# Kernel optimization log

Hardware: AMD Instinct MI355X
Metric: run time of the kernel (lower is better)

The kernel has to match this reference:

```python
import jax, jax.numpy as jnp
import numpy as np

N, IN_F, OUT_F, G = 8192, 1024, 1024, 5


def setup_inputs() -> dict:
    key = jax.random.key(0)
    k1, k2 = jax.random.split(key)
    x = jax.random.normal(k1, (N, IN_F), dtype=jnp.float32)
    spline_weights = jax.random.normal(k2, (OUT_F, IN_F, G), dtype=jnp.float32) * 0.1
    return {"x": x, "spline_weights": spline_weights}


def reference(x, spline_weights):
    out_f, in_f, g = spline_weights.shape
    grid = jnp.linspace(-1.0, 1.0, g).astype(x.dtype)
    leading = x.shape[:-1]
    xf = x.reshape(-1, in_f)                       # [N, in]
    x_c = jnp.clip(jnp.tanh(xf), grid[0], grid[-1])
    # bucket index: number of grid points <= x_c, minus 1, clamped to [0, g-2]
    idx = jnp.sum(x_c[..., None] >= grid, axis=-1) - 1
    idx = jnp.clip(idx, 0, g - 2)                  # [N, in] int
    idx_r = jnp.minimum(idx + 1, g - 1)
    g_left = grid[idx]
    g_right = grid[idx_r]
    t = (x_c - g_left) / (g_right - g_left + 1e-8)  # [N, in]
    # sparse interpolation coefficients over the grid axis: two nonzeros per (n,i)
    oh_l = jax.nn.one_hot(idx, g, dtype=xf.dtype)   # [N, in, G]
    oh_r = jax.nn.one_hot(idx_r, g, dtype=xf.dtype)
    coeff = (1.0 - t)[..., None] * oh_l + t[..., None] * oh_r  # [N, in, G]
    # y[n,o] = sum_i (1-t) * W[o,i,idx] + t * W[o,i,idx+1]
    out = jnp.einsum('nig,oig->no', coeff, spline_weights)
    return out.reshape(*leading, out_f)
```

## Files before the change

kernel.cpp:

```cpp
#include <hip/hip_runtime.h>
#include <stdint.h>

#define N_ROWS 8192
#define IN_F   1024
#define OUT_F  1024
#define NG     5
#define KTOT   (IN_F * NG)

typedef float          f32x4 __attribute__((ext_vector_type(4)));
typedef short          s16x8 __attribute__((ext_vector_type(8)));
typedef unsigned short u16x8 __attribute__((ext_vector_type(8)));

__device__ __forceinline__ unsigned short f2bf_rne(float f) {
    unsigned u = __float_as_uint(f);
    u = (u + 0x7fffu + ((u >> 16) & 1u)) >> 16;
    return (unsigned short)u;
}
__device__ __forceinline__ float bf2f(unsigned short h) {
    return __uint_as_float(((unsigned)h) << 16);
}
__device__ __forceinline__ void gload_lds16(const void* g, void* l) {
    __builtin_amdgcn_global_load_lds(
        (const __attribute__((address_space(1))) unsigned int*)g,
        (__attribute__((address_space(3))) unsigned int*)l, 16, 0, 0);
}

__global__ __launch_bounds__(256) void prep_a(const float* __restrict__ x,
                                              unsigned short* __restrict__ Ahp,
                                              unsigned short* __restrict__ Alp) {
    int t = blockIdx.x * 256 + threadIdx.x;
    int n = t >> 7, i8 = t & 127;
    const float4* xp = reinterpret_cast<const float4*>(x + (size_t)n * IN_F + i8 * 8);
    float4 a = xp[0], b = xp[1];
    float r[8] = {a.x, a.y, a.z, a.w, b.x, b.y, b.z, b.w};
    float xc[8];
#pragma unroll
    for (int j = 0; j < 8; ++j) {
        float v = fminf(fmaxf(r[j], -9.0f), 9.0f);
        float e = __expf(2.0f * v);
        xc[j] = (e - 1.0f) / (e + 1.0f);
    }
    size_t base = (size_t)n * KTOT + i8 * 8;
#pragma unroll
    for (int g = 0; g < NG; ++g) {
        float gv = -1.0f + 0.5f * (float)g;
        u16x8 hv, lv;
#pragma unroll
        for (int j = 0; j < 8; ++j) {
            float c  = fmaxf(0.0f, fmaf(-2.0f, fabsf(xc[j] - gv), 1.0f));
            unsigned hb = __float_as_uint(c) >> 16;
            hv[j] = (unsigned short)hb;
            lv[j] = (unsigned short)(__float_as_uint(c - __uint_as_float(hb << 16)) >> 16);
        }
        *reinterpret_cast<u16x8*>(&Ahp[base + g * 1024]) = hv;
        *reinterpret_cast<u16x8*>(&Alp[base + g * 1024]) = lv;
    }
}

__global__ __launch_bounds__(256) void prep_w(const float* __restrict__ W,
                                              unsigned short* __restrict__ Wh,
                                              unsigned short* __restrict__ Wl) {
    int t  = blockIdx.x * 256 + threadIdx.x;
    int o  = t >> 8, i4 = (t & 255) * 4;
    const float4* wp = reinterpret_cast<const float4*>(W + (size_t)o * KTOT + i4 * NG);
    float f[20];
#pragma unroll
    for (int q = 0; q < 5; ++q) {
        float4 v = wp[q];
        f[q*4+0] = v.x; f[q*4+1] = v.y; f[q*4+2] = v.z; f[q*4+3] = v.w;
    }
#pragma unroll
    for (int g = 0; g < NG; ++g) {
        ushort4 hq, lq;
        unsigned short* hp = (unsigned short*)&hq;
        unsigned short* lp = (unsigned short*)&lq;
#pragma unroll
        for (int di = 0; di < 4; ++di) {
            float w = f[di * NG + g];
            unsigned short h = f2bf_rne(w);
            hp[di] = h;
            lp[di] = f2bf_rne(w - bf2f(h));
        }
        int dst = o * KTOT + g * 1024 + i4;
        *reinterpret_cast<ushort4*>(&Wh[dst]) = hq;
        *reinterpret_cast<ushort4*>(&Wl[dst]) = lq;
    }
}

#define BM 128
#define BN 128
#define PBK 32
#define PNKT (KTOT / PBK)

struct SLdsDB { unsigned short d[2][4][BM * PBK]; };

__global__ __launch_bounds__(256, 2) void kan_gemm_pure(
        const unsigned short* __restrict__ Ahp,
        const unsigned short* __restrict__ Alp,
        const unsigned short* __restrict__ Wh,
        const unsigned short* __restrict__ Wl,
        float* __restrict__ out) {
    __shared__ SLdsDB s;

    int bid = blockIdx.x;
    int wg  = (bid & 7) * 64 + (bid >> 3);
    int nb  = wg >> 6;
    int mb  = wg & 63;
    int n0 = mb * BM, o0 = nb * BN;

    int tid  = threadIdx.x;
    int lane = tid & 63, wid = tid >> 6;
    int wm = wid >> 1, wn = wid & 1;

    int ks = (lane & 3) ^ ((lane >> 3) & 3);
    int gA[2], gB[2], ldsb[2];
#pragma unroll
    for (int q = 0; q < 2; ++q) {
        int r = wid * 32 + q * 16 + (lane >> 2);
        gA[q] = (n0 + r) * KTOT + ks * 8;
        gB[q] = (o0 + r) * KTOT + ks * 8;
        ldsb[q] = (wid * 32 + q * 16) * PBK;
    }
    int sl0  = lane >> 4;
    int arow = wm * 64 + (lane & 15);
    int brow = wn * 64 + (lane & 15);
    int aaddr = arow * PBK + ((sl0 ^ ((arow >> 1) & 3)) << 3);
    int baddr = brow * PBK + ((sl0 ^ ((brow >> 1) & 3)) << 3);

    f32x4 acc[4][4] = {};

    auto STAGE = [&](int buf, int k0) {
#pragma unroll
        for (int q = 0; q < 2; ++q) {
            gload_lds16(Ahp + gA[q] + k0, &s.d[buf][0][ldsb[q]]);
            gload_lds16(Alp + gA[q] + k0, &s.d[buf][1][ldsb[q]]);
            gload_lds16(Wh  + gB[q] + k0, &s.d[buf][2][ldsb[q]]);
            gload_lds16(Wl  + gB[q] + k0, &s.d[buf][3][ldsb[q]]);
        }
    };
    auto COMPUTE = [&](int buf) {
        s16x8 ah[4], al[4], bh[4], bl[4];
#pragma unroll
        for (int m = 0; m < 4; ++m) {
            ah[m] = *reinterpret_cast<const s16x8*>(&s.d[buf][0][aaddr + m * 512]);
            al[m] = *reinterpret_cast<const s16x8*>(&s.d[buf][1][aaddr + m * 512]);
        }
#pragma unroll
        for (int nf = 0; nf < 4; ++nf) {
            bh[nf] = *reinterpret_cast<const s16x8*>(&s.d[buf][2][baddr + nf * 512]);
            bl[nf] = *reinterpret_cast<const s16x8*>(&s.d[buf][3][baddr + nf * 512]);
        }
#pragma unroll
        for (int m = 0; m < 4; ++m)
#pragma unroll
            for (int nf = 0; nf < 4; ++nf) {
                acc[m][nf] = __builtin_amdgcn_mfma_f32_16x16x32_bf16(
                                 ah[m], bh[nf], acc[m][nf], 0, 0, 0);
                acc[m][nf] = __builtin_amdgcn_mfma_f32_16x16x32_bf16(
                                 ah[m], bl[nf], acc[m][nf], 0, 0, 0);
                acc[m][nf] = __builtin_amdgcn_mfma_f32_16x16x32_bf16(
                                 al[m], bh[nf], acc[m][nf], 0, 0, 0);
            }
    };

    STAGE(0, 0);
    __syncthreads();
    int cur = 0;
    for (int kt = 0; kt < PNKT - 1; ++kt) {
        STAGE(cur ^ 1, (kt + 1) * PBK);
        COMPUTE(cur);
        __syncthreads();
        cur ^= 1;
    }
    COMPUTE(cur);

    int rb = n0 + wm * 64 + (lane >> 4) * 4;
    int cb = o0 + wn * 64 + (lane & 15);
#pragma unroll
    for (int m = 0; m < 4; ++m)
#pragma unroll
        for (int nf = 0; nf < 4; ++nf)
#pragma unroll
            for (int jj = 0; jj < 4; ++jj)
                out[(size_t)(rb + m * 16 + jj) * OUT_F + cb + nf * 16] =
                    acc[m][nf][jj];
}

__global__ __launch_bounds__(256) void prep_p(const float* __restrict__ x,
                                              unsigned short* __restrict__ P) {
    int t = blockIdx.x * 256 + threadIdx.x;
    float4 a = reinterpret_cast<const float4*>(x)[t * 2];
    float4 b = reinterpret_cast<const float4*>(x)[t * 2 + 1];
    float r[8] = {a.x, a.y, a.z, a.w, b.x, b.y, b.z, b.w};
    u16x8 o;
#pragma unroll
    for (int j = 0; j < 8; ++j) {
        float xc = fminf(fmaxf(r[j], -9.0f), 9.0f);
        float e  = __expf(2.0f * xc);
        float th = (e - 1.0f) / (e + 1.0f);
        o[j] = (unsigned short)__float2uint_rn((th + 1.0f) * 32767.0f);
    }
    *reinterpret_cast<u16x8*>(&P[(size_t)t * 8]) = o;
}

#define MBM 64
#define MBN 256
#define MBK 32
struct SLdsM {
    unsigned short Ah[4 * MBM * 8];
    unsigned short Al[4 * MBM * 8];
    unsigned short Bh[4 * MBN * 8];
    unsigned short Bl[4 * MBN * 8];
};

__global__ __launch_bounds__(256, 3) void kan_gemm_mid(
        const unsigned short* __restrict__ P,
        const unsigned short* __restrict__ Wh,
        const unsigned short* __restrict__ Wl,
        float* __restrict__ out) {
    __shared__ SLdsM s;
    int bid = blockIdx.x;
    int wg  = (bid & 7) * 64 + (bid >> 3);
    int nb  = wg >> 7, mb = wg & 127;
    int n0 = mb * MBM, o0 = nb * MBN;
    int tid  = threadIdx.x;
    int lane = tid & 63, w = tid >> 6;

    int arow = tid >> 2, aks = tid & 3;
    int agoff = (n0 + arow) * IN_F + aks * 8;
    int aldst = aks * (MBM * 8) + arow * 8;
    int brow4 = tid >> 2, bchunk = tid & 3;
    int bldst = bchunk * (MBN * 8) + brow4 * 8;
    int bgq[4];
#pragma unroll
    for (int q = 0; q < 4; ++q)
        bgq[q] = (o0 + q * 64 + brow4) * KTOT + bchunk * 8;
    int fchunk = lane >> 4, fr = lane & 15;

    f32x4 acc[4][4] = {};
    for (int kt = 0; kt < KTOT / MBK; ++kt) {
        int k0 = kt * MBK;
        float gv = -1.0f + 0.5f * (float)(kt >> 5);
        int i0 = (kt & 31) * MBK;
        __syncthreads();
        u16x8 bregh[4], bregl[4];
#pragma unroll
        for (int q = 0; q < 4; ++q)
            bregh[q] = *reinterpret_cast<const u16x8*>(&Wh[bgq[q] + k0]);
#pragma unroll
        for (int q = 0; q < 4; ++q)
            bregl[q] = *reinterpret_cast<const u16x8*>(&Wl[bgq[q] + k0]);
        {
            u16x8 u = *reinterpret_cast<const u16x8*>(&P[agoff + i0]);
            u16x8 hv, lv;
#pragma unroll
            for (int j = 0; j < 8; ++j) {
                float xc = fmaf((float)u[j], (1.0f / 32767.0f), -1.0f);
                float c  = fmaxf(0.0f, fmaf(-2.0f, fabsf(xc - gv), 1.0f));
                unsigned hb = __float_as_uint(c) >> 16;
                hv[j] = (unsigned short)hb;
                lv[j] = (unsigned short)(__float_as_uint(c - __uint_as_float(hb << 16)) >> 16);
            }
            *reinterpret_cast<u16x8*>(&s.Ah[aldst]) = hv;
            *reinterpret_cast<u16x8*>(&s.Al[aldst]) = lv;
        }
#pragma unroll
        for (int q = 0; q < 4; ++q) {
            *reinterpret_cast<u16x8*>(&s.Bh[bldst + q * 512]) = bregh[q];
            *reinterpret_cast<u16x8*>(&s.Bl[bldst + q * 512]) = bregl[q];
        }
        __syncthreads();

        s16x8 ah[4], al[4], bh[4], bl[4];
#pragma unroll
        for (int m = 0; m < 4; ++m) {
            int e = fchunk * (MBM * 8) + (m * 16 + fr) * 8;
            ah[m] = *reinterpret_cast<const s16x8*>(&s.Ah[e]);
            al[m] = *reinterpret_cast<const s16x8*>(&s.Al[e]);
        }
#pragma unroll
        for (int nf = 0; nf < 4; ++nf) {
            int e = fchunk * (MBN * 8) + (w * 64 + nf * 16 + fr) * 8;
            bh[nf] = *reinterpret_cast<const s16x8*>(&s.Bh[e]);
            bl[nf] = *reinterpret_cast<const s16x8*>(&s.Bl[e]);
        }
#pragma unroll
        for (int m = 0; m < 4; ++m)
#pragma unroll
            for (int nf = 0; nf < 4; ++nf) {
                acc[m][nf] = __builtin_amdgcn_mfma_f32_16x16x32_bf16(
                                 ah[m], bh[nf], acc[m][nf], 0, 0, 0);
                acc[m][nf] = __builtin_amdgcn_mfma_f32_16x16x32_bf16(
                                 ah[m], bl[nf], acc[m][nf], 0, 0, 0);
                acc[m][nf] = __builtin_amdgcn_mfma_f32_16x16x32_bf16(
                                 al[m], bh[nf], acc[m][nf], 0, 0, 0);
            }
    }
    int rb = n0 + (lane >> 4) * 4;
    int cb = o0 + w * 64 + (lane & 15);
#pragma unroll
    for (int m = 0; m < 4; ++m)
#pragma unroll
        for (int nf = 0; nf < 4; ++nf)
#pragma unroll
            for (int jj = 0; jj < 4; ++jj)
                out[(size_t)(rb + m * 16 + jj) * OUT_F + cb + nf * 16] =
                    acc[m][nf][jj];
}

__global__ __launch_bounds__(256) void kan_naive(const float* __restrict__ x,
                                                 const float* __restrict__ W,
                                                 float* __restrict__ out) {
    int bn = blockIdx.x & 3;
    int bm = blockIdx.x >> 2;
    int o = bn * 256 + threadIdx.x;
    int nbase = bm * 16;
    float acc[16];
#pragma unroll
    for (int j = 0; j < 16; ++j) acc[j] = 0.0f;
    for (int i = 0; i < IN_F; ++i) {
        const float* wp = &W[(size_t)o * KTOT + i * NG];
        float w0 = wp[0], w1 = wp[1], w2 = wp[2], w3 = wp[3], w4 = wp[4];
#pragma unroll
        for (int j = 0; j < 16; ++j) {
            float xc = tanhf(x[(size_t)(nbase + j) * IN_F + i]);
            float c0 = fmaxf(0.f, fmaf(-2.f, fabsf(xc + 1.0f), 1.f));
            float c1 = fmaxf(0.f, fmaf(-2.f, fabsf(xc + 0.5f), 1.f));
            float c2 = fmaxf(0.f, fmaf(-2.f, fabsf(xc), 1.f));
            float c3 = fmaxf(0.f, fmaf(-2.f, fabsf(xc - 0.5f), 1.f));
            float c4 = fmaxf(0.f, fmaf(-2.f, fabsf(xc - 1.0f), 1.f));
            acc[j] += c0 * w0 + c1 * w1 + c2 * w2 + c3 * w3 + c4 * w4;
        }
    }
#pragma unroll
    for (int j = 0; j < 16; ++j)
        out[(size_t)(nbase + j) * OUT_F + o] = acc[j];
}

extern "C" void kernel_launch(void* const* d_in, const int* in_sizes, int n_in,
                              void* d_out, int out_size, void* d_ws, size_t ws_size,
                              hipStream_t stream) {
    const float* x = (const float*)d_in[0];
    const float* W = (const float*)d_in[1];
    float* out = (float*)d_out;

    const size_t APLANE  = (size_t)N_ROWS * KTOT * 2;
    const size_t WPLANE  = (size_t)OUT_F * KTOT * 2;
    const size_t P_BYTES = (size_t)N_ROWS * IN_F * 2;

    if (ws_size >= 2 * APLANE + 2 * WPLANE) {
        unsigned short* Ahp = (unsigned short*)d_ws;
        unsigned short* Alp = (unsigned short*)((char*)d_ws + APLANE);
        unsigned short* Wh  = (unsigned short*)((char*)d_ws + 2 * APLANE);
        unsigned short* Wl  = (unsigned short*)((char*)d_ws + 2 * APLANE + WPLANE);
        prep_a<<<(N_ROWS * IN_F / 8) / 256, 256, 0, stream>>>(x, Ahp, Alp);
        prep_w<<<(OUT_F * IN_F / 4) / 256, 256, 0, stream>>>(W, Wh, Wl);
        kan_gemm_pure<<<512, 256, 0, stream>>>(Ahp, Alp, Wh, Wl, out);
    } else if (ws_size >= P_BYTES + 2 * WPLANE) {
        unsigned short* P  = (unsigned short*)d_ws;
        unsigned short* Wh = (unsigned short*)((char*)d_ws + P_BYTES);
        unsigned short* Wl = (unsigned short*)((char*)d_ws + P_BYTES + WPLANE);
        prep_p<<<(N_ROWS * IN_F / 8) / 256, 256, 0, stream>>>(x, P);
        prep_w<<<(OUT_F * IN_F / 4) / 256, 256, 0, stream>>>(W, Wh, Wl);
        kan_gemm_mid<<<512, 256, 0, stream>>>(P, Wh, Wl, out);
    } else {
        kan_naive<<<2048, 256, 0, stream>>>(x, W, out);
    }
}
```

Before: 374.9 us.

## Drop materialized A planes; build spline coeffs in-kernel from quantized tanh

Removes the path that writes the full hi/lo bf16 coefficient planes for A, which is about 168MB of intermediate traffic. The default path now uses the mid kernel, which expands the 16-bit quantized tanh values into coefficients inside the GEMM. The mid kernel also gains register prefetch of the next K tile, overlapping global loads with the MFMA work, and its occupancy hint drops from 3 to 2. The trade-off is extra per-tile ALU work and single-buffered LDS with two barriers per iteration instead of async LDS loads.

```diff
diff --git a/kernel.cpp b/kernel.cpp
--- a/kernel.cpp
+++ b/kernel.cpp
@@ -19,42 +19,22 @@
 __device__ __forceinline__ float bf2f(unsigned short h) {
     return __uint_as_float(((unsigned)h) << 16);
 }
-__device__ __forceinline__ void gload_lds16(const void* g, void* l) {
-    __builtin_amdgcn_global_load_lds(
-        (const __attribute__((address_space(1))) unsigned int*)g,
-        (__attribute__((address_space(3))) unsigned int*)l, 16, 0, 0);
-}
-
-__global__ __launch_bounds__(256) void prep_a(const float* __restrict__ x,
-                                              unsigned short* __restrict__ Ahp,
-                                              unsigned short* __restrict__ Alp) {
+
+__global__ __launch_bounds__(256) void prep_p(const float* __restrict__ x,
+                                              unsigned short* __restrict__ P) {
     int t = blockIdx.x * 256 + threadIdx.x;
-    int n = t >> 7, i8 = t & 127;
-    const float4* xp = reinterpret_cast<const float4*>(x + (size_t)n * IN_F + i8 * 8);
-    float4 a = xp[0], b = xp[1];
+    float4 a = reinterpret_cast<const float4*>(x)[t * 2];
+    float4 b = reinterpret_cast<const float4*>(x)[t * 2 + 1];
     float r[8] = {a.x, a.y, a.z, a.w, b.x, b.y, b.z, b.w};
-    float xc[8];
+    u16x8 o;
 #pragma unroll
     for (int j = 0; j < 8; ++j) {
-        float v = fminf(fmaxf(r[j], -9.0f), 9.0f);
-        float e = __expf(2.0f * v);
-        xc[j] = (e - 1.0f) / (e + 1.0f);
-    }
-    size_t base = (size_t)n * KTOT + i8 * 8;
-#pragma unroll
-    for (int g = 0; g < NG; ++g) {
-        float gv = -1.0f + 0.5f * (float)g;
-        u16x8 hv, lv;
-#pragma unroll
-        for (int j = 0; j < 8; ++j) {
-            float c  = fmaxf(0.0f, fmaf(-2.0f, fabsf(xc[j] - gv), 1.0f));
-            unsigned hb = __float_as_uint(c) >> 16;
-            hv[j] = (unsigned short)hb;
-            lv[j] = (unsigned short)(__float_as_uint(c - __uint_as_float(hb << 16)) >> 16);
-        }
-        *reinterpret_cast<u16x8*>(&Ahp[base + g * 1024]) = hv;
-        *reinterpret_cast<u16x8*>(&Alp[base + g * 1024]) = lv;
-    }
+        float xc = fminf(fmaxf(r[j], -9.0f), 9.0f);
+        float e  = __expf(2.0f * xc);
+        float th = (e - 1.0f) / (e + 1.0f);
+        o[j] = (unsigned short)__float2uint_rn((th + 1.0f) * 32767.0f);
+    }
+    *reinterpret_cast<u16x8*>(&P[(size_t)t * 8]) = o;
 }
 
 __global__ __launch_bounds__(256) void prep_w(const float* __restrict__ W,
@@ -87,68 +67,102 @@
     }
 }
 
-#define BM 128
-#define BN 128
-#define PBK 32
-#define PNKT (KTOT / PBK)
-
-struct SLdsDB { unsigned short d[2][4][BM * PBK]; };
-
-__global__ __launch_bounds__(256, 2) void kan_gemm_pure(
-        const unsigned short* __restrict__ Ahp,
-        const unsigned short* __restrict__ Alp,
+#define MBM 64
+#define MBN 256
+#define MBK 32
+#define MNKT (KTOT / MBK)
+
+struct SLdsM {
+    unsigned short Ah[4 * MBM * 8];
+    unsigned short Al[4 * MBM * 8];
+    unsigned short Bh[4 * MBN * 8];
+    unsigned short Bl[4 * MBN * 8];
+};
+
+__global__ __launch_bounds__(256, 2) void kan_gemm_mid(
+        const unsigned short* __restrict__ P,
         const unsigned short* __restrict__ Wh,
         const unsigned short* __restrict__ Wl,
         float* __restrict__ out) {
-    __shared__ SLdsDB s;
+    __shared__ SLdsM s;
 
     int bid = blockIdx.x;
     int wg  = (bid & 7) * 64 + (bid >> 3);
-    int nb  = wg >> 6;
-    int mb  = wg & 63;
-    int n0 = mb * BM, o0 = nb * BN;
+    int nb  = wg >> 7, mb = wg & 127;
+    int n0 = mb * MBM, o0 = nb * MBN;
 
     int tid  = threadIdx.x;
-    int lane = tid & 63, wid = tid >> 6;
-    int wm = wid >> 1, wn = wid & 1;
-
-    int ks = (lane & 3) ^ ((lane >> 3) & 3);
-    int gA[2], gB[2], ldsb[2];
-#pragma unroll
-    for (int q = 0; q < 2; ++q) {
-        int r = wid * 32 + q * 16 + (lane >> 2);
-        gA[q] = (n0 + r) * KTOT + ks * 8;
-        gB[q] = (o0 + r) * KTOT + ks * 8;
-        ldsb[q] = (wid * 32 + q * 16) * PBK;
-    }
-    int sl0  = lane >> 4;
-    int arow = wm * 64 + (lane & 15);
-    int brow = wn * 64 + (lane & 15);
-    int aaddr = arow * PBK + ((sl0 ^ ((arow >> 1) & 3)) << 3);
-    int baddr = brow * PBK + ((sl0 ^ ((brow >> 1) & 3)) << 3);
+    int lane = tid & 63, w = tid >> 6;
+
+    int arow = tid >> 2, aks = tid & 3;
+    int agoff = (n0 + arow) * IN_F + aks * 8;
+    int aldst = aks * (MBM * 8) + arow * 8;
+    int brow4 = tid >> 2, bchunk = tid & 3;
+    int bldst = bchunk * (MBN * 8) + brow4 * 8;
+    int bgq[4];
+#pragma unroll
+    for (int q = 0; q < 4; ++q)
+        bgq[q] = (o0 + q * 64 + brow4) * KTOT + bchunk * 8;
+    int fchunk = lane >> 4, fr = lane & 15;
 
     f32x4 acc[4][4] = {};
 
-    auto STAGE = [&](int buf, int k0) {
-#pragma unroll
-        for (int q = 0; q < 2; ++q) {
-            gload_lds16(Ahp + gA[q] + k0, &s.d[buf][0][ldsb[q]]);
-            gload_lds16(Alp + gA[q] + k0, &s.d[buf][1][ldsb[q]]);
-            gload_lds16(Wh  + gB[q] + k0, &s.d[buf][2][ldsb[q]]);
-            gload_lds16(Wl  + gB[q] + k0, &s.d[buf][3][ldsb[q]]);
-        }
-    };
-    auto COMPUTE = [&](int buf) {
+    u16x8 bregh[4], bregl[4], uP;
+#pragma unroll
+    for (int q = 0; q < 4; ++q) bregh[q] = *reinterpret_cast<const u16x8*>(&Wh[bgq[q]]);
+#pragma unroll
+    for (int q = 0; q < 4; ++q) bregl[q] = *reinterpret_cast<const u16x8*>(&Wl[bgq[q]]);
+    uP = *reinterpret_cast<const u16x8*>(&P[agoff]);
+
+    for (int kt = 0; kt < MNKT; ++kt) {
+        float gv = -1.0f + 0.5f * (float)(kt >> 5);
+
+        __syncthreads();
+
+        {
+            u16x8 hv, lv;
+#pragma unroll
+            for (int j = 0; j < 8; ++j) {
+                float xc = fmaf((float)uP[j], (1.0f / 32767.0f), -1.0f);
+                float c  = fmaxf(0.0f, fmaf(-2.0f, fabsf(xc - gv), 1.0f));
+                unsigned hb = __float_as_uint(c) >> 16;
+                hv[j] = (unsigned short)hb;
+                lv[j] = (unsigned short)(__float_as_uint(c - __uint_as_float(hb << 16)) >> 16);
+            }
+            *reinterpret_cast<u16x8*>(&s.Ah[aldst]) = hv;
+            *reinterpret_cast<u16x8*>(&s.Al[aldst]) = lv;
+        }
+#pragma unroll
+        for (int q = 0; q < 4; ++q) {
+            *reinterpret_cast<u16x8*>(&s.Bh[bldst + q * 512]) = bregh[q];
+            *reinterpret_cast<u16x8*>(&s.Bl[bldst + q * 512]) = bregl[q];
+        }
+        __syncthreads();
+
+        if (kt + 1 < MNKT) {
+            int k0n = (kt + 1) * MBK;
+            int i0n = ((kt + 1) & 31) * MBK;
+#pragma unroll
+            for (int q = 0; q < 4; ++q)
+                bregh[q] = *reinterpret_cast<const u16x8*>(&Wh[bgq[q] + k0n]);
+#pragma unroll
+            for (int q = 0; q < 4; ++q)
+                bregl[q] = *reinterpret_cast<const u16x8*>(&Wl[bgq[q] + k0n]);
+            uP = *reinterpret_cast<const u16x8*>(&P[agoff + i0n]);
+        }
+
         s16x8 ah[4], al[4], bh[4], bl[4];
 #pragma unroll
         for (int m = 0; m < 4; ++m) {
-            ah[m] = *reinterpret_cast<const s16x8*>(&s.d[buf][0][aaddr + m * 512]);
-            al[m] = *reinterpret_cast<const s16x8*>(&s.d[buf][1][aaddr + m * 512]);
+            int e = fchunk * (MBM * 8) + (m * 16 + fr) * 8;
+            ah[m] = *reinterpret_cast<const s16x8*>(&s.Ah[e]);
+            al[m] = *reinterpret_cast<const s16x8*>(&s.Al[e]);
         }
 #pragma unroll
         for (int nf = 0; nf < 4; ++nf) {
-            bh[nf] = *reinterpret_cast<const s16x8*>(&s.d[buf][2][baddr + nf * 512]);
-            bl[nf] = *reinterpret_cast<const s16x8*>(&s.d[buf][3][baddr + nf * 512]);
+            int e = fchunk * (MBN * 8) + (w * 64 + nf * 16 + fr) * 8;
+            bh[nf] = *reinterpret_cast<const s16x8*>(&s.Bh[e]);
+            bl[nf] = *reinterpret_cast<const s16x8*>(&s.Bl[e]);
         }
 #pragma unroll
         for (int m = 0; m < 4; ++m)
@@ -161,141 +175,8 @@
                 acc[m][nf] = __builtin_amdgcn_mfma_f32_16x16x32_bf16(
                                  al[m], bh[nf], acc[m][nf], 0, 0, 0);
             }
-    };
-
-    STAGE(0, 0);
-    __syncthreads();
-    int cur = 0;
-    for (int kt = 0; kt < PNKT - 1; ++kt) {
-        STAGE(cur ^ 1, (kt + 1) * PBK);
-        COMPUTE(cur);
-        __syncthreads();
-        cur ^= 1;
-    }
-    COMPUTE(cur);
-
-    int rb = n0 + wm * 64 + (lane >> 4) * 4;
-    int cb = o0 + wn * 64 + (lane & 15);
-#pragma unroll
-    for (int m = 0; m < 4; ++m)
-#pragma unroll
-        for (int nf = 0; nf < 4; ++nf)
-#pragma unroll
-            for (int jj = 0; jj < 4; ++jj)
-                out[(size_t)(rb + m * 16 + jj) * OUT_F + cb + nf * 16] =
-                    acc[m][nf][jj];
-}
-
-__global__ __launch_bounds__(256) void prep_p(const float* __restrict__ x,
-                                              unsigned short* __restrict__ P) {
-    int t = blockIdx.x * 256 + threadIdx.x;
-    float4 a = reinterpret_cast<const float4*>(x)[t * 2];
-    float4 b = reinterpret_cast<const float4*>(x)[t * 2 + 1];
-    float r[8] = {a.x, a.y, a.z, a.w, b.x, b.y, b.z, b.w};
-    u16x8 o;
-#pragma unroll
-    for (int j = 0; j < 8; ++j) {
-        float xc = fminf(fmaxf(r[j], -9.0f), 9.0f);
-        float e  = __expf(2.0f * xc);
-        float th = (e - 1.0f) / (e + 1.0f);
-        o[j] = (unsigned short)__float2uint_rn((th + 1.0f) * 32767.0f);
-    }
-    *reinterpret_cast<u16x8*>(&P[(size_t)t * 8]) = o;
-}
-
-#define MBM 64
-#define MBN 256
-#define MBK 32
-struct SLdsM {
-    unsigned short Ah[4 * MBM * 8];
-    unsigned short Al[4 * MBM * 8];
-    unsigned short Bh[4 * MBN * 8];
-    unsigned short Bl[4 * MBN * 8];
-};
-
-__global__ __launch_bounds__(256, 3) void kan_gemm_mid(
-        const unsigned short* __restrict__ P,
-        const unsigned short* __restrict__ Wh,
-        const unsigned short* __restrict__ Wl,
-        float* __restrict__ out) {
-    __shared__ SLdsM s;
-    int bid = blockIdx.x;
-    int wg  = (bid & 7) * 64 + (bid >> 3);
-    int nb  = wg >> 7, mb = wg & 127;
-    int n0 = mb * MBM, o0 = nb * MBN;
-    int tid  = threadIdx.x;
-    int lane = tid & 63, w = tid >> 6;
-
-    int arow = tid >> 2, aks = tid & 3;
-    int agoff = (n0 + arow) * IN_F + aks * 8;
-    int aldst = aks * (MBM * 8) + arow * 8;
-    int brow4 = tid >> 2, bchunk = tid & 3;
-    int bldst = bchunk * (MBN * 8) + brow4 * 8;
-    int bgq[4];
-#pragma unroll
-    for (int q = 0; q < 4; ++q)
-        bgq[q] = (o0 + q * 64 + brow4) * KTOT + bchunk * 8;
-    int fchunk = lane >> 4, fr = lane & 15;
-
-    f32x4 acc[4][4] = {};
-    for (int kt = 0; kt < KTOT / MBK; ++kt) {
-        int k0 = kt * MBK;
-        float gv = -1.0f + 0.5f * (float)(kt >> 5);
-        int i0 = (kt & 31) * MBK;
-        __syncthreads();
-        u16x8 bregh[4], bregl[4];
-#pragma unroll
-        for (int q = 0; q < 4; ++q)
-            bregh[q] = *reinterpret_cast<const u16x8*>(&Wh[bgq[q] + k0]);
-#pragma unroll
-        for (int q = 0; q < 4; ++q)
-            bregl[q] = *reinterpret_cast<const u16x8*>(&Wl[bgq[q] + k0]);
-        {
-            u16x8 u = *reinterpret_cast<const u16x8*>(&P[agoff + i0]);
-            u16x8 hv, lv;
-#pragma unroll
-            for (int j = 0; j < 8; ++j) {
-                float xc = fmaf((float)u[j], (1.0f / 32767.0f), -1.0f);
-                float c  = fmaxf(0.0f, fmaf(-2.0f, fabsf(xc - gv), 1.0f));
-                unsigned hb = __float_as_uint(c) >> 16;
-                hv[j] = (unsigned short)hb;
-                lv[j] = (unsigned short)(__float_as_uint(c - __uint_as_float(hb << 16)) >> 16);
-            }
-            *reinterpret_cast<u16x8*>(&s.Ah[aldst]) = hv;
-            *reinterpret_cast<u16x8*>(&s.Al[aldst]) = lv;
-        }
-#pragma unroll
-        for (int q = 0; q < 4; ++q) {
-            *reinterpret_cast<u16x8*>(&s.Bh[bldst + q * 512]) = bregh[q];
-            *reinterpret_cast<u16x8*>(&s.Bl[bldst + q * 512]) = bregl[q];
-        }
-        __syncthreads();
-
-        s16x8 ah[4], al[4], bh[4], bl[4];
-#pragma unroll
-        for (int m = 0; m < 4; ++m) {
-            int e = fchunk * (MBM * 8) + (m * 16 + fr) * 8;
-            ah[m] = *reinterpret_cast<const s16x8*>(&s.Ah[e]);
-            al[m] = *reinterpret_cast<const s16x8*>(&s.Al[e]);
-        }
-#pragma unroll
-        for (int nf = 0; nf < 4; ++nf) {
-            int e = fchunk * (MBN * 8) + (w * 64 + nf * 16 + fr) * 8;
-            bh[nf] = *reinterpret_cast<const s16x8*>(&s.Bh[e]);
-            bl[nf] = *reinterpret_cast<const s16x8*>(&s.Bl[e]);
-        }
-#pragma unroll
-        for (int m = 0; m < 4; ++m)
-#pragma unroll
-            for (int nf = 0; nf < 4; ++nf) {
-                acc[m][nf] = __builtin_amdgcn_mfma_f32_16x16x32_bf16(
-                                 ah[m], bh[nf], acc[m][nf], 0, 0, 0);
-                acc[m][nf] = __builtin_amdgcn_mfma_f32_16x16x32_bf16(
-                                 ah[m], bl[nf], acc[m][nf], 0, 0, 0);
-                acc[m][nf] = __builtin_amdgcn_mfma_f32_16x16x32_bf16(
-                                 al[m], bh[nf], acc[m][nf], 0, 0, 0);
-            }
-    }
+    }
+
     int rb = n0 + (lane >> 4) * 4;
     int cb = o0 + w * 64 + (lane & 15);
 #pragma unroll
@@ -344,19 +225,10 @@
     const float* W = (const float*)d_in[1];
     float* out = (float*)d_out;
 
-    const size_t APLANE  = (size_t)N_ROWS * KTOT * 2;
+    const size_t P_BYTES = (size_t)N_ROWS * IN_F * 2;
     const size_t WPLANE  = (size_t)OUT_F * KTOT * 2;
-    const size_t P_BYTES = (size_t)N_ROWS * IN_F * 2;
-
-    if (ws_size >= 2 * APLANE + 2 * WPLANE) {
-        unsigned short* Ahp = (unsigned short*)d_ws;
-        unsigned short* Alp = (unsigned short*)((char*)d_ws + APLANE);
-        unsigned short* Wh  = (unsigned short*)((char*)d_ws + 2 * APLANE);
-        unsigned short* Wl  = (unsigned short*)((char*)d_ws + 2 * APLANE + WPLANE);
-        prep_a<<<(N_ROWS * IN_F / 8) / 256, 256, 0, stream>>>(x, Ahp, Alp);
-        prep_w<<<(OUT_F * IN_F / 4) / 256, 256, 0, stream>>>(W, Wh, Wl);
-        kan_gemm_pure<<<512, 256, 0, stream>>>(Ahp, Alp, Wh, Wl, out);
-    } else if (ws_size >= P_BYTES + 2 * WPLANE) {
+
+    if (ws_size >= P_BYTES + 2 * WPLANE) {
         unsigned short* P  = (unsigned short*)d_ws;
         unsigned short* Wh = (unsigned short*)((char*)d_ws + P_BYTES);
         unsigned short* Wl = (unsigned short*)((char*)d_ws + P_BYTES + WPLANE);
```

Result: slower. 410.1 us (+9.4%).
